# Optimization experiments

Hardware: AMD Instinct MI355X
Metric: run time of the kernel (lower is better)

Reference implementation:

```python
import jax, jax.numpy as jnp
import numpy as np

T, D, FF, E, K = 512, 2048, 768, 128, 8


def setup_inputs() -> dict:
    key = jax.random.key(0)
    k0, k1, k2, k3, k4 = jax.random.split(key, 5)
    scale = 0.02
    return {
        "hidden_states": jax.random.normal(k0, (T, D), dtype=jnp.float32),
        "w_gate": jax.random.normal(k1, (D, E), dtype=jnp.float32) * scale,  # router
        "w_gate_proj": jax.random.normal(k2, (E, D, FF), dtype=jnp.float32) * scale,
        "w_up_proj": jax.random.normal(k3, (E, D, FF), dtype=jnp.float32) * scale,
        "w_down_proj": jax.random.normal(k4, (E, FF, D), dtype=jnp.float32) * scale,
    }


def reference(hidden_states, w_gate, w_gate_proj, w_up_proj, w_down_proj):
    x = hidden_states  # [T, D]
    # Router: linear -> softmax (fp32) -> top-k -> renormalize (norm_topk_prob=True)
    router_logits = jnp.dot(x, w_gate)  # [T, E]
    probs = jax.nn.softmax(router_logits.astype(jnp.float32), axis=-1)
    topk_w, topk_idx = jax.lax.top_k(probs, K)  # [T, K]
    topk_w = topk_w / jnp.sum(topk_w, axis=-1, keepdims=True)
    topk_w = topk_w.astype(x.dtype)
    # Scatter per-(token,expert) combine weights: [T, E]
    rows = jnp.arange(T)[:, None]
    combine = jnp.zeros((T, E), dtype=x.dtype).at[rows, topk_idx].add(topk_w)
    # Grouped SwiGLU experts: scan over experts, weighted accumulation.
    def body(acc, per_expert):
        wg, wu, wd, s = per_expert  # [D,FF], [D,FF], [FF,D], [T]
        h = jax.nn.silu(jnp.dot(x, wg)) * jnp.dot(x, wu)  # [T, FF]
        return acc + s[:, None] * jnp.dot(h, wd), None

    init = jnp.zeros_like(x)
    out, _ = jax.lax.scan(
        body, init, (w_gate_proj, w_up_proj, w_down_proj, combine.T)
    )
    return out  # [T, D]
```

## Files before the change

### kernel.cpp

```cpp
#include <hip/hip_runtime.h>
#include <hip/hip_bf16.h>

#define TT 512
#define DH 2048
#define FFD 768
#define NE 128
#define TOPK 8
#define CAP 512
#define SMAX 64

typedef __attribute__((ext_vector_type(4))) float f32x4;
typedef __attribute__((ext_vector_type(8))) short short8;

typedef __attribute__((address_space(3))) unsigned int lds_u32_t;
typedef __attribute__((address_space(1))) unsigned int glob_u32_t;

__device__ __forceinline__ short f2bf(float f) {
    __hip_bfloat16 h = __float2bfloat16(f);
    return *reinterpret_cast<short*>(&h);
}

__device__ __forceinline__ void glds16(const float* g, float* l) {
    __builtin_amdgcn_global_load_lds((glob_u32_t*)g, (lds_u32_t*)l, 16, 0, 0);
}

template<int N>
__device__ __forceinline__ void vmwait() {
    asm volatile("s_waitcnt vmcnt(%0)" :: "i"(N) : "memory");
}

__global__ __launch_bounds__(128) void moe_init(int* __restrict__ cnt)
{
    cnt[threadIdx.x] = 0;
}

__global__ __launch_bounds__(128) void moe_router(
    const float* __restrict__ x, const float* __restrict__ wg,
    int* __restrict__ cnt, int* __restrict__ tok_list, float* __restrict__ w_list,
    float* __restrict__ out)
{
    const int t = blockIdx.x;
    const int e = threadIdx.x;
    __shared__ float xs[DH];
    __shared__ float red[NE];
    __shared__ int   redi[NE];
    __shared__ float selw[TOPK];
    __shared__ int   seli[TOPK];

    float4* outrow = (float4*)(out + (size_t)t * DH);
    const float4 z4 = make_float4(0.f, 0.f, 0.f, 0.f);
    #pragma unroll
    for (int i = 0; i < 4; ++i) outrow[e + i * 128] = z4;

    for (int i = e; i < DH; i += 128) xs[i] = x[(size_t)t * DH + i];
    __syncthreads();

    float acc = 0.f;
    #pragma unroll 4
    for (int d = 0; d < DH; ++d)
        acc = fmaf(xs[d], wg[(size_t)d * NE + e], acc);

    red[e] = acc; __syncthreads();
    for (int s = 64; s > 0; s >>= 1) {
        if (e < s) red[e] = fmaxf(red[e], red[e + s]);
        __syncthreads();
    }
    const float mx = red[0];
    __syncthreads();

    float myp = __expf(acc - mx);

    for (int k = 0; k < TOPK; ++k) {
        red[e] = myp; redi[e] = e;
        __syncthreads();
        for (int s = 64; s > 0; s >>= 1) {
            if (e < s) {
                const float v2 = red[e + s]; const int i2 = redi[e + s];
                if (v2 > red[e] || (v2 == red[e] && i2 < redi[e])) { red[e] = v2; redi[e] = i2; }
            }
            __syncthreads();
        }
        if (e == 0) { selw[k] = red[0]; seli[k] = redi[0]; }
        __syncthreads();
        if (e == seli[k]) myp = -1.f;
        __syncthreads();
    }

    if (e == 0) {
        float s8 = 0.f;
        #pragma unroll
        for (int k = 0; k < TOPK; ++k) s8 += selw[k];
        const float inv = 1.f / s8;
        #pragma unroll
        for (int k = 0; k < TOPK; ++k) {
            const int ex = seli[k];
            const float wv = selw[k] * inv;
            const int pos = atomicAdd(&cnt[ex], 1);
            if (pos < CAP) {
                tok_list[ex * CAP + pos] = t * TOPK + k;
                w_list[ex * CAP + pos] = wv;
            }
        }
    }
}

__global__ __launch_bounds__(256) void moe_gather(
    const float* __restrict__ x, const int* __restrict__ cnt,
    const int* __restrict__ tok_list, short* __restrict__ xgb)
{
    const int e = blockIdx.x;
    int n = cnt[e]; if (n > SMAX) n = SMAX;
    const int k = threadIdx.x * 8;
    short* dste = xgb + (size_t)e * SMAX * DH;
    for (int s = 0; s < SMAX; ++s) {
        short8 o = {0, 0, 0, 0, 0, 0, 0, 0};
        if (s < n) {
            const float* xr = x + (size_t)(tok_list[e * CAP + s] >> 3) * DH + k;
            const float4 v0 = *(const float4*)(xr);
            const float4 v1 = *(const float4*)(xr + 4);
            o[0] = f2bf(v0.x); o[1] = f2bf(v0.y); o[2] = f2bf(v0.z); o[3] = f2bf(v0.w);
            o[4] = f2bf(v1.x); o[5] = f2bf(v1.y); o[6] = f2bf(v1.z); o[7] = f2bf(v1.w);
        }
        *(short8*)(dste + (size_t)s * DH + k) = o;
    }
}

__global__ __launch_bounds__(64) void moe_gateup(
    const short* __restrict__ xgb,
    const float* __restrict__ wgp, const float* __restrict__ wup,
    short* __restrict__ hc)
{
    __shared__ __align__(16) float Bsh[6 * 2048];

    const int e = blockIdx.y;
    const int lane = threadIdx.x;
    const int fl = lane & 15;
    const int g16 = lane >> 4;
    const int koff = g16 * 8;
    const int f0 = blockIdx.x * 64;
    const int lrow = lane >> 4;
    const int lcol = (lane & 15) * 4;

    const short* xge = xgb + (size_t)e * SMAX * DH;
    const float* wgs = wgp + (size_t)e * DH * FFD + f0;
    const float* wus = wup + (size_t)e * DH * FFD + f0;

    f32x4 accg[4][4] = {};
    f32x4 accu[4][4] = {};
    short8 A0[4], A1[4], A2[4];

    auto ISSUE = [&](int t, int buf) {
        const int kk = t * 32;
        float* bg = &Bsh[buf * 2048];
        float* bu = &Bsh[6144 + buf * 2048];
        #pragma unroll
        for (int g = 0; g < 8; ++g) {
            const size_t ro = (size_t)(kk + g * 4 + lrow) * FFD + lcol;
            glds16(wgs + ro, bg + g * 256);
            glds16(wus + ro, bu + g * 256);
        }
    };
    auto LOADA = [&](int t, short8 (&a)[4]) {
        const int kk = t * 32 + koff;
        #pragma unroll
        for (int fm = 0; fm < 4; ++fm)
            a[fm] = *(const short8*)(xge + (size_t)(fm * 16 + fl) * DH + kk);
    };
    auto COMP = [&](int buf, const short8 (&a)[4]) {
        const float* bg = &Bsh[buf * 2048 + koff * 64 + fl];
        const float* bu = &Bsh[6144 + buf * 2048 + koff * 64 + fl];
        #pragma unroll
        for (int nf = 0; nf < 4; ++nf) {
            short8 bfg, bfu;
            #pragma unroll
            for (int j = 0; j < 8; ++j) {
                bfg[j] = f2bf(bg[nf * 16 + j * 64]);
                bfu[j] = f2bf(bu[nf * 16 + j * 64]);
            }
            #pragma unroll
            for (int fm = 0; fm < 4; ++fm) {
                accg[nf][fm] = __builtin_amdgcn_mfma_f32_16x16x32_bf16(a[fm], bfg, accg[nf][fm], 0, 0, 0);
                accu[nf][fm] = __builtin_amdgcn_mfma_f32_16x16x32_bf16(a[fm], bfu, accu[nf][fm], 0, 0, 0);
            }
        }
    };

    LOADA(0, A0); ISSUE(0, 0);
    LOADA(1, A1); ISSUE(1, 1);
    for (int i = 0; i < 20; ++i) {
        const int t = 3 * i;
        LOADA(t + 2, A2); ISSUE(t + 2, 2); vmwait<40>(); COMP(0, A0);
        LOADA(t + 3, A0); ISSUE(t + 3, 0); vmwait<40>(); COMP(1, A1);
        LOADA(t + 4, A1); ISSUE(t + 4, 1); vmwait<40>(); COMP(2, A2);
    }
    LOADA(62, A2); ISSUE(62, 2); vmwait<40>(); COMP(0, A0);
    LOADA(63, A0); ISSUE(63, 0); vmwait<40>(); COMP(1, A1);
    vmwait<20>(); COMP(2, A2);
    vmwait<0>();  COMP(0, A0);

    short* hce = hc + (size_t)e * SMAX * FFD + f0;
    #pragma unroll
    for (int nf = 0; nf < 4; ++nf) {
        #pragma unroll
        for (int fm = 0; fm < 4; ++fm) {
            #pragma unroll
            for (int r = 0; r < 4; ++r) {
                const int s = fm * 16 + g16 * 4 + r;
                const float g = accg[nf][fm][r];
                const float u = accu[nf][fm][r];
                const float hv = (g / (1.f + __expf(-g))) * u;
                hce[(size_t)s * FFD + nf * 16 + fl] = f2bf(hv);
            }
        }
    }
}

__global__ __launch_bounds__(64) void moe_down(
    const short* __restrict__ hc, const float* __restrict__ wdp,
    const int* __restrict__ cnt, const int* __restrict__ tok_list,
    const float* __restrict__ w_list, float* __restrict__ out)
{
    __shared__ __align__(16) float Bsh[3 * 2048];

    const int e = blockIdx.y;
    int n = cnt[e]; if (n > SMAX) n = SMAX;
    if (n == 0) return;

    const int lane = threadIdx.x;
    const int fl = lane & 15;
    const int g16 = lane >> 4;
    const int koff = g16 * 8;
    const int d0 = blockIdx.x * 64;
    const int lrow = lane >> 4;
    const int lcol = (lane & 15) * 4;

    const short* hce = hc + (size_t)e * SMAX * FFD;
    const float* wds = wdp + (size_t)e * FFD * DH + d0;

    f32x4 acc[4][4] = {};
    short8 A0[4], A1[4], A2[4];

    auto ISSUE = [&](int t, int buf) {
        const int kk = t * 32;
        float* bd = &Bsh[buf * 2048];
        #pragma unroll
        for (int g = 0; g < 8; ++g) {
            const size_t ro = (size_t)(kk + g * 4 + lrow) * DH + lcol;
            glds16(wds + ro, bd + g * 256);
        }
    };
    auto LOADA = [&](int t, short8 (&a)[4]) {
        const int kk = t * 32 + koff;
        #pragma unroll
        for (int fm = 0; fm < 4; ++fm)
            a[fm] = *(const short8*)(hce + (size_t)(fm * 16 + fl) * FFD + kk);
    };
    auto COMP = [&](int buf, const short8 (&a)[4]) {
        const float* bp = &Bsh[buf * 2048 + koff * 64 + fl];
        #pragma unroll
        for (int nf = 0; nf < 4; ++nf) {
            short8 bf;
            #pragma unroll
            for (int j = 0; j < 8; ++j) bf[j] = f2bf(bp[nf * 16 + j * 64]);
            #pragma unroll
            for (int fm = 0; fm < 4; ++fm)
                acc[nf][fm] = __builtin_amdgcn_mfma_f32_16x16x32_bf16(a[fm], bf, acc[nf][fm], 0, 0, 0);
        }
    };

    LOADA(0, A0); ISSUE(0, 0);
    LOADA(1, A1); ISSUE(1, 1);
    for (int i = 0; i < 6; ++i) {
        const int t = 3 * i;
        LOADA(t + 2, A2); ISSUE(t + 2, 2); vmwait<24>(); COMP(0, A0);
        LOADA(t + 3, A0); ISSUE(t + 3, 0); vmwait<24>(); COMP(1, A1);
        LOADA(t + 4, A1); ISSUE(t + 4, 1); vmwait<24>(); COMP(2, A2);
    }
    LOADA(20, A2); ISSUE(20, 2); vmwait<24>(); COMP(0, A0);
    LOADA(21, A0); ISSUE(21, 0); vmwait<24>(); COMP(1, A1);
    LOADA(22, A1); ISSUE(22, 1); vmwait<24>(); COMP(2, A2);
    LOADA(23, A2); ISSUE(23, 2); vmwait<24>(); COMP(0, A0);
    vmwait<12>(); COMP(1, A1);
    vmwait<0>();  COMP(2, A2);

    #pragma unroll
    for (int nf = 0; nf < 4; ++nf) {
        #pragma unroll
        for (int fm = 0; fm < 4; ++fm) {
            #pragma unroll
            for (int r = 0; r < 4; ++r) {
                const int s = fm * 16 + g16 * 4 + r;
                if (s < n) {
                    const int t = tok_list[e * CAP + s] >> 3;
                    const float wt = w_list[e * CAP + s];
                    atomicAdd(out + (size_t)t * DH + d0 + nf * 16 + fl, acc[nf][fm][r] * wt);
                }
            }
        }
    }
}

extern "C" void kernel_launch(void* const* d_in, const int* in_sizes, int n_in,
                              void* d_out, int out_size, void* d_ws, size_t ws_size,
                              hipStream_t stream) {
    const float* x   = (const float*)d_in[0];
    const float* wg  = (const float*)d_in[1];
    const float* wgp = (const float*)d_in[2];
    const float* wup = (const float*)d_in[3];
    const float* wdp = (const float*)d_in[4];
    float* out = (float*)d_out;

    char* ws = (char*)d_ws;
    int*   cnt      = (int*)ws;
    int*   tok_list = (int*)(ws + 1024);
    float* w_list   = (float*)(ws + 1024 + NE * CAP * 4);
    short* xgb      = (short*)(ws + (1 << 20));
    short* hc       = (short*)(ws + (1 << 20) + (size_t)NE * SMAX * DH * 2);

    moe_init<<<1, 128, 0, stream>>>(cnt);
    moe_router<<<TT, 128, 0, stream>>>(x, wg, cnt, tok_list, w_list, out);
    moe_gather<<<NE, 256, 0, stream>>>(x, cnt, tok_list, xgb);
    moe_gateup<<<dim3(FFD / 64, NE), 64, 0, stream>>>(xgb, wgp, wup, hc);
    moe_down<<<dim3(DH / 64, NE), 64, 0, stream>>>(hc, wdp, cnt, tok_list, w_list, out);
}
```

Before: 777.1 us.

## Split gate/up projections across two waves and use double buffering

The gate-up kernel now runs two waves per block. One wave computes the gate projection and the other the up projection, each with its own LDS buffers. The gate accumulators are then exchanged through LDS so the second wave can apply SiLU and write the product. This halves per-wave accumulator registers and weight-streaming work, aiming at better occupancy and latency hiding. Both the gate-up and down kernels move from triple to double buffering of the weight tiles, which cuts LDS use but leaves less prefetch depth to hide global-load latency.

```diff
diff --git a/kernel.cpp b/kernel.cpp
--- a/kernel.cpp
+++ b/kernel.cpp
@@ -125,15 +125,17 @@
     }
 }
 
-__global__ __launch_bounds__(64) void moe_gateup(
+__global__ __launch_bounds__(128) void moe_gateup(
     const short* __restrict__ xgb,
     const float* __restrict__ wgp, const float* __restrict__ wup,
     short* __restrict__ hc)
 {
-    __shared__ __align__(16) float Bsh[6 * 2048];
+    __shared__ __align__(16) float Bsh[2 * 2 * 2048];
 
     const int e = blockIdx.y;
-    const int lane = threadIdx.x;
+    const int tid = threadIdx.x;
+    const int lane = tid & 63;
+    const int wv = tid >> 6;
     const int fl = lane & 15;
     const int g16 = lane >> 4;
     const int koff = g16 * 8;
@@ -142,22 +144,20 @@
     const int lcol = (lane & 15) * 4;
 
     const short* xge = xgb + (size_t)e * SMAX * DH;
-    const float* wgs = wgp + (size_t)e * DH * FFD + f0;
-    const float* wus = wup + (size_t)e * DH * FFD + f0;
-
-    f32x4 accg[4][4] = {};
-    f32x4 accu[4][4] = {};
-    short8 A0[4], A1[4], A2[4];
+    const float* wsrc = (wv == 0 ? wgp : wup) + (size_t)e * DH * FFD + f0;
+
+    float* myB = &Bsh[wv * 4096];
+
+    f32x4 acc[4][4] = {};
+    short8 aA[4], aB[4];
 
     auto ISSUE = [&](int t, int buf) {
         const int kk = t * 32;
-        float* bg = &Bsh[buf * 2048];
-        float* bu = &Bsh[6144 + buf * 2048];
+        float* b = myB + buf * 2048;
         #pragma unroll
         for (int g = 0; g < 8; ++g) {
             const size_t ro = (size_t)(kk + g * 4 + lrow) * FFD + lcol;
-            glds16(wgs + ro, bg + g * 256);
-            glds16(wus + ro, bu + g * 256);
+            glds16(wsrc + ro, b + g * 256);
         }
     };
     auto LOADA = [&](int t, short8 (&a)[4]) {
@@ -167,51 +167,55 @@
             a[fm] = *(const short8*)(xge + (size_t)(fm * 16 + fl) * DH + kk);
     };
     auto COMP = [&](int buf, const short8 (&a)[4]) {
-        const float* bg = &Bsh[buf * 2048 + koff * 64 + fl];
-        const float* bu = &Bsh[6144 + buf * 2048 + koff * 64 + fl];
+        const float* bp = myB + buf * 2048 + koff * 64 + fl;
         #pragma unroll
         for (int nf = 0; nf < 4; ++nf) {
-            short8 bfg, bfu;
-            #pragma unroll
-            for (int j = 0; j < 8; ++j) {
-                bfg[j] = f2bf(bg[nf * 16 + j * 64]);
-                bfu[j] = f2bf(bu[nf * 16 + j * 64]);
-            }
-            #pragma unroll
-            for (int fm = 0; fm < 4; ++fm) {
-                accg[nf][fm] = __builtin_amdgcn_mfma_f32_16x16x32_bf16(a[fm], bfg, accg[nf][fm], 0, 0, 0);
-                accu[nf][fm] = __builtin_amdgcn_mfma_f32_16x16x32_bf16(a[fm], bfu, accu[nf][fm], 0, 0, 0);
-            }
-        }
-    };
-
-    LOADA(0, A0); ISSUE(0, 0);
-    LOADA(1, A1); ISSUE(1, 1);
-    for (int i = 0; i < 20; ++i) {
-        const int t = 3 * i;
-        LOADA(t + 2, A2); ISSUE(t + 2, 2); vmwait<40>(); COMP(0, A0);
-        LOADA(t + 3, A0); ISSUE(t + 3, 0); vmwait<40>(); COMP(1, A1);
-        LOADA(t + 4, A1); ISSUE(t + 4, 1); vmwait<40>(); COMP(2, A2);
-    }
-    LOADA(62, A2); ISSUE(62, 2); vmwait<40>(); COMP(0, A0);
-    LOADA(63, A0); ISSUE(63, 0); vmwait<40>(); COMP(1, A1);
-    vmwait<20>(); COMP(2, A2);
-    vmwait<0>();  COMP(0, A0);
-
-    short* hce = hc + (size_t)e * SMAX * FFD + f0;
-    #pragma unroll
-    for (int nf = 0; nf < 4; ++nf) {
-        #pragma unroll
-        for (int fm = 0; fm < 4; ++fm) {
-            #pragma unroll
-            for (int r = 0; r < 4; ++r) {
-                const int s = fm * 16 + g16 * 4 + r;
-                const float g = accg[nf][fm][r];
-                const float u = accu[nf][fm][r];
-                const float hv = (g / (1.f + __expf(-g))) * u;
-                hce[(size_t)s * FFD + nf * 16 + fl] = f2bf(hv);
-            }
-        }
+            short8 bf;
+            #pragma unroll
+            for (int j = 0; j < 8; ++j) bf[j] = f2bf(bp[nf * 16 + j * 64]);
+            #pragma unroll
+            for (int fm = 0; fm < 4; ++fm)
+                acc[nf][fm] = __builtin_amdgcn_mfma_f32_16x16x32_bf16(a[fm], bf, acc[nf][fm], 0, 0, 0);
+        }
+    };
+
+    ISSUE(0, 0); LOADA(0, aA);
+    for (int t = 0; t < 63; ++t) {
+        ISSUE(t + 1, (t + 1) & 1);
+        if (t & 1) LOADA(t + 1, aA); else LOADA(t + 1, aB);
+        vmwait<12>();
+        if (t & 1) COMP(1, aB); else COMP(0, aA);
+    }
+    vmwait<0>();
+    COMP(1, aB);
+
+    float* G = Bsh;
+    if (wv == 0) {
+        #pragma unroll
+        for (int nf = 0; nf < 4; ++nf)
+            #pragma unroll
+            for (int fm = 0; fm < 4; ++fm)
+                #pragma unroll
+                for (int r = 0; r < 4; ++r) {
+                    const int s = fm * 16 + g16 * 4 + r;
+                    G[s * 64 + nf * 16 + fl] = acc[nf][fm][r];
+                }
+    }
+    __syncthreads();
+    if (wv == 1) {
+        short* hce = hc + (size_t)e * SMAX * FFD + f0;
+        #pragma unroll
+        for (int nf = 0; nf < 4; ++nf)
+            #pragma unroll
+            for (int fm = 0; fm < 4; ++fm)
+                #pragma unroll
+                for (int r = 0; r < 4; ++r) {
+                    const int s = fm * 16 + g16 * 4 + r;
+                    const float g = G[s * 64 + nf * 16 + fl];
+                    const float u = acc[nf][fm][r];
+                    const float hv = (g / (1.f + __expf(-g))) * u;
+                    hce[(size_t)s * FFD + nf * 16 + fl] = f2bf(hv);
+                }
     }
 }
 
@@ -220,7 +224,7 @@
     const int* __restrict__ cnt, const int* __restrict__ tok_list,
     const float* __restrict__ w_list, float* __restrict__ out)
 {
-    __shared__ __align__(16) float Bsh[3 * 2048];
+    __shared__ __align__(16) float Bsh[2 * 2048];
 
     const int e = blockIdx.y;
     int n = cnt[e]; if (n > SMAX) n = SMAX;
@@ -238,7 +242,7 @@
     const float* wds = wdp + (size_t)e * FFD * DH + d0;
 
     f32x4 acc[4][4] = {};
-    short8 A0[4], A1[4], A2[4];
+    short8 aA[4], aB[4];
 
     auto ISSUE = [&](int t, int buf) {
         const int kk = t * 32;
@@ -268,20 +272,15 @@
         }
     };
 
-    LOADA(0, A0); ISSUE(0, 0);
-    LOADA(1, A1); ISSUE(1, 1);
-    for (int i = 0; i < 6; ++i) {
-        const int t = 3 * i;
-        LOADA(t + 2, A2); ISSUE(t + 2, 2); vmwait<24>(); COMP(0, A0);
-        LOADA(t + 3, A0); ISSUE(t + 3, 0); vmwait<24>(); COMP(1, A1);
-        LOADA(t + 4, A1); ISSUE(t + 4, 1); vmwait<24>(); COMP(2, A2);
-    }
-    LOADA(20, A2); ISSUE(20, 2); vmwait<24>(); COMP(0, A0);
-    LOADA(21, A0); ISSUE(21, 0); vmwait<24>(); COMP(1, A1);
-    LOADA(22, A1); ISSUE(22, 1); vmwait<24>(); COMP(2, A2);
-    LOADA(23, A2); ISSUE(23, 2); vmwait<24>(); COMP(0, A0);
-    vmwait<12>(); COMP(1, A1);
-    vmwait<0>();  COMP(2, A2);
+    ISSUE(0, 0); LOADA(0, aA);
+    for (int t = 0; t < 23; ++t) {
+        ISSUE(t + 1, (t + 1) & 1);
+        if (t & 1) LOADA(t + 1, aA); else LOADA(t + 1, aB);
+        vmwait<12>();
+        if (t & 1) COMP(1, aB); else COMP(0, aA);
+    }
+    vmwait<0>();
+    COMP(1, aB);
 
     #pragma unroll
     for (int nf = 0; nf < 4; ++nf) {
@@ -320,6 +319,6 @@
     moe_init<<<1, 128, 0, stream>>>(cnt);
     moe_router<<<TT, 128, 0, stream>>>(x, wg, cnt, tok_list, w_list, out);
     moe_gather<<<NE, 256, 0, stream>>>(x, cnt, tok_list, xgb);
-    moe_gateup<<<dim3(FFD / 64, NE), 64, 0, stream>>>(xgb, wgp, wup, hc);
+    moe_gateup<<<dim3(FFD / 64, NE), 128, 0, stream>>>(xgb, wgp, wup, hc);
     moe_down<<<dim3(DH / 64, NE), 64, 0, stream>>>(hc, wdp, cnt, tok_list, w_list, out);
 }
```

Result: slower. 856.3 us (+10.2%).
